# Performance work log

Measured on AMD Instinct MI355X. Metric: run time of the kernel, lower is better.

## Reference

```python
import jax, jax.numpy as jnp
import numpy as np


def setup_inputs() -> dict:
    key = jax.random.key(0)
    k1, k2, k3 = jax.random.split(key, 3)
    B, T, C = 4, 2048, 1024
    dim = C
    x = jax.random.normal(k1, (B, T, C), dtype=jnp.float32)
    # torch nn.Linear weight layout: [out_features, in_features], scaled like kaiming-uniform-ish
    w_qkv = jax.random.normal(k2, (3 * dim, dim), dtype=jnp.float32) * (1.0 / np.sqrt(dim))
    w_out = jax.random.normal(k3, (dim, dim), dtype=jnp.float32) * (1.0 / np.sqrt(dim))
    return {"x": x, "w_qkv": w_qkv, "w_out": w_out}


def reference(x, w_qkv, w_out):
    B, T, C = x.shape
    n_heads = 16
    head_dim = C // n_heads

    qkv = jnp.einsum("btc,dc->btd", x, w_qkv)  # [B,T,3C]
    q, k, v = jnp.split(qkv, 3, axis=-1)

    def split_heads(t):
        return t.reshape(B, T, n_heads, head_dim).transpose(0, 2, 1, 3)  # [B,H,T,hd]

    q, k, v = split_heads(q), split_heads(k), split_heads(v)

    scale = 1.0 / np.sqrt(head_dim).astype(np.float32)
    scores = jnp.einsum("bhqd,bhkd->bhqk", q, k) * scale  # [B,H,T,T]
    causal = jnp.tril(jnp.ones((T, T), dtype=bool))
    scores = jnp.where(causal, scores, jnp.finfo(scores.dtype).min)
    attn = jax.nn.softmax(scores, axis=-1)
    out = jnp.einsum("bhqk,bhkd->bhqd", attn, v)  # [B,H,T,hd]
    out = out.transpose(0, 2, 1, 3).reshape(B, T, C)
    return jnp.einsum("btc,dc->btd", out, w_out)
```

## Files before the change

kernel.cpp:

```cpp
#include <hip/hip_runtime.h>
#include <hip/hip_bf16.h>


typedef __attribute__((ext_vector_type(8))) short bf16x8;
typedef __attribute__((ext_vector_type(4))) float f32x4;
typedef __attribute__((ext_vector_type(16))) float f32x16;
typedef __attribute__((ext_vector_type(2))) unsigned uint2v;

#define GLOBAL_AS __attribute__((address_space(1)))
#define LDS_AS __attribute__((address_space(3)))

__device__ __forceinline__ unsigned short f2b_rne(float f) {
  unsigned u = __float_as_uint(f);
  unsigned r = u + 0x7fffu + ((u >> 16) & 1u);
  return (unsigned short)(r >> 16);
}

__device__ __forceinline__ unsigned cvt_pk_bf16(float lo, float hi) {
  unsigned r;
  asm("v_cvt_pk_bf16_f32 %0, %1, %2" : "=v"(r) : "v"(lo), "v"(hi));
  return r;
}

__device__ __forceinline__ void gload_lds16(const void* g, void* l) {
  __builtin_amdgcn_global_load_lds((const GLOBAL_AS void*)g, (LDS_AS void*)l, 16, 0, 0);
}

__global__ void f32_to_bf16_vec(const float* __restrict__ src,
                                unsigned short* __restrict__ dst, int n4) {
  int i = blockIdx.x * blockDim.x + threadIdx.x;
  int stride = gridDim.x * blockDim.x;
  for (; i < n4; i += stride) {
    float4 v = reinterpret_cast<const float4*>(src)[i];
    ushort4 o;
    o.x = f2b_rne(v.x); o.y = f2b_rne(v.y);
    o.z = f2b_rne(v.z); o.w = f2b_rne(v.w);
    reinterpret_cast<ushort4*>(dst)[i] = o;
  }
}

__global__ __launch_bounds__(256)
void v_transpose(const unsigned short* __restrict__ qkv,
                 unsigned short* __restrict__ vt) {
  __shared__ __align__(16) unsigned short Ts[64][64];
  const int tc = blockIdx.x, bh = blockIdx.y;
  const int b = bh >> 4, hed = bh & 15;
  const int t0 = tc * 64;
  const int tid = threadIdx.x;
  {
    const int r = tid >> 2, cb = (tid & 3) * 2;
    const unsigned short* src =
        qkv + (size_t)(b * 2048 + t0 + r) * 3072 + 2048 + hed * 64;
    bf16x8 v0 = *(const bf16x8*)(src + cb * 8);
    bf16x8 v1 = *(const bf16x8*)(src + cb * 8 + 8);
    *(bf16x8*)&Ts[r][(cb ^ (r & 7)) * 8] = v0;
    *(bf16x8*)&Ts[r][((cb + 1) ^ (r & 7)) * 8] = v1;
  }
  __syncthreads();
  const int d = tid >> 2;
  unsigned short* dst = vt + ((size_t)bh * 64 + d) * 2048 + t0;
#pragma unroll
  for (int tb2 = 0; tb2 < 2; ++tb2) {
    int tb = (tid & 3) * 2 + tb2;
    union { unsigned short s[8]; bf16x8 v; } o;
#pragma unroll
    for (int i = 0; i < 8; ++i) {
      int row = tb * 8 + i;
      o.s[i] = Ts[row][(((d >> 3) ^ (row & 7)) * 8) + (d & 7)];
    }
    *(bf16x8*)(dst + tb * 8) = o.v;
  }
}

template <int N, int OUT_BF16>
__global__ __launch_bounds__(512)
void gemm_big(const unsigned short* __restrict__ A,
              const unsigned short* __restrict__ B,
              void* __restrict__ Cout) {
  const int K = 1024;
  __shared__ __align__(16) unsigned short As[2][2][128 * 64];
  __shared__ __align__(16) unsigned short Bs[2][128 * 64];

  const int tid = threadIdx.x, wid = tid >> 6, lane = tid & 63;
  const int l31 = lane & 31, h = lane >> 5;
  const int NBX = N / 128;
  const int nwg8 = (int)gridDim.x >> 3;
  const int wgid = ((int)blockIdx.x & 7) * nwg8 + ((int)blockIdx.x >> 3);
  const int bx = wgid % NBX, by = wgid / NBX;
  const int m0 = by * 256, n0 = bx * 128;
  const int wr = wid >> 1, wc = wid & 1;

  auto stage = [&](int t, int buf) {
    const int k0 = t * 64;
    const int r8 = lane >> 3;
    const int blk = (lane & 7) ^ r8;
#pragma unroll
    for (int hh = 0; hh < 2; ++hh)
#pragma unroll
      for (int r = 0; r < 2; ++r) {
        int row = r * 64 + wid * 8 + r8;
        gload_lds16(A + (size_t)(m0 + hh * 128 + row) * K + k0 + blk * 8,
                    &As[buf][hh][r * 4096 + wid * 512]);
      }
#pragma unroll
    for (int r = 0; r < 2; ++r) {
      int row = r * 64 + wid * 8 + r8;
      gload_lds16(B + (size_t)(n0 + row) * K + k0 + blk * 8,
                  &Bs[buf][r * 4096 + wid * 512]);
    }
  };

  f32x16 acc[2][2] = {};

  stage(0, 0);

  int cur = 0;
  for (int t = 0; t < 16; ++t) {
    __builtin_amdgcn_s_barrier();
    if (t + 1 < 16) {
      stage(t + 1, cur ^ 1);
      asm volatile("s_waitcnt vmcnt(6)" ::: "memory");
    } else {
      asm volatile("s_waitcnt vmcnt(0)" ::: "memory");
    }
    __builtin_amdgcn_s_barrier();
    __builtin_amdgcn_sched_barrier(0);

    bf16x8 af[2][4], bfr[2][4];
#pragma unroll
    for (int mi = 0; mi < 2; ++mi) {
      int row = (wr & 1) * 64 + mi * 32 + l31;
#pragma unroll
      for (int ks = 0; ks < 4; ++ks) {
        int chunk = (ks * 2 + h) ^ (row & 7);
        af[mi][ks] = *(const bf16x8*)&As[cur][wr >> 1][row * 64 + chunk * 8];
      }
    }
#pragma unroll
    for (int ni = 0; ni < 2; ++ni) {
      int row = wc * 64 + ni * 32 + l31;
#pragma unroll
      for (int ks = 0; ks < 4; ++ks) {
        int chunk = (ks * 2 + h) ^ (row & 7);
        bfr[ni][ks] = *(const bf16x8*)&Bs[cur][row * 64 + chunk * 8];
      }
    }
    __builtin_amdgcn_s_setprio(1);
#pragma unroll
    for (int ks = 0; ks < 4; ++ks)
#pragma unroll
      for (int mi = 0; mi < 2; ++mi)
#pragma unroll
        for (int ni = 0; ni < 2; ++ni)
          acc[mi][ni] = __builtin_amdgcn_mfma_f32_32x32x16_bf16(
              af[mi][ks], bfr[ni][ks], acc[mi][ni], 0, 0, 0);
    __builtin_amdgcn_s_setprio(0);
    cur ^= 1;
  }

#pragma unroll
  for (int mi = 0; mi < 2; ++mi)
#pragma unroll
    for (int ni = 0; ni < 2; ++ni)
#pragma unroll
      for (int reg = 0; reg < 16; ++reg) {
        int row = m0 + wr * 64 + mi * 32 + (reg & 3) + 8 * (reg >> 2) + 4 * h;
        int col = n0 + wc * 64 + ni * 32 + l31;
        if (OUT_BF16)
          ((unsigned short*)Cout)[(size_t)row * N + col] =
              f2b_rne(acc[mi][ni][reg]);
        else
          ((float*)Cout)[(size_t)row * N + col] = acc[mi][ni][reg];
      }
}

__global__ __launch_bounds__(256, 2)
void attn_fwd(const unsigned short* __restrict__ qkv,
              const unsigned short* __restrict__ vt,
              unsigned short* __restrict__ out) {
  const int T = 2048, C3 = 3072;
  __shared__ __align__(16) unsigned short Ks[2][64][64];
  __shared__ __align__(16) unsigned short Vs[2][64][64];
  __shared__ float Bc[4][32];

  const int tid = threadIdx.x, w = tid >> 6, lane = tid & 63;
  const int l31 = lane & 31, h = lane >> 5;
  const int wgid = (blockIdx.x & 7) * 64 + (blockIdx.x >> 3);
  const int local = wgid & 63, xcd = wgid >> 6;
  const int qidx = local >> 3, bhl = local & 7;
  const int bh = xcd * 8 + bhl;
  const int qt = (qidx < 4) ? (7 - qidx) : (qidx - 4);
  const int b = bh >> 4, hed = bh & 15;
  const int qw = qt * 256 + w * 64;
  const size_t rowbase = (size_t)b * T * C3;
  const int hoff = hed * 64;
  const unsigned short* vbase = vt + (size_t)bh * 64 * 2048;
  const float c2 = 0.18033688f;

  auto stageK = [&](int kv0, int buf) {
#pragma unroll
    for (int pp = 0; pp < 2; ++pp) {
      int chunk = w * 2 + pp;
      int row = chunk * 8 + (lane >> 3);
      int blk = (lane & 7) ^ (lane >> 3);
      gload_lds16(
          qkv + rowbase + (size_t)(kv0 + row) * C3 + 1024 + hoff + blk * 8,
          &Ks[buf][chunk * 8][0]);
    }
  };
  auto stageV = [&](int kv0, int buf) {
#pragma unroll
    for (int pp = 0; pp < 2; ++pp) {
      int chunk = w * 2 + pp;
      int drow = chunk * 8 + (lane >> 3);
      int blk = (lane & 7) ^ (lane >> 3);
      gload_lds16(vbase + (size_t)drow * 2048 + kv0 + blk * 8,
                  &Vs[buf][chunk * 8][0]);
    }
  };

  bf16x8 qf0[4], qf1[4];
  {
    const unsigned short* qp0 =
        qkv + rowbase + (size_t)(qw + l31) * C3 + hoff + h * 8;
    const unsigned short* qp1 = qp0 + 32 * C3;
#pragma unroll
    for (int s = 0; s < 4; ++s) {
      qf0[s] = *(const bf16x8*)(qp0 + 16 * s);
      qf1[s] = *(const bf16x8*)(qp1 + 16 * s);
    }
  }

  f32x16 oacc0[2] = {}, oacc1[2] = {};
  float mr0 = -1e30f, mr1 = -1e30f, sum0 = 0.f, sum1 = 0.f;

  stageK(0, 0);
  stageV(0, 0);

  auto do_half = [&](f32x16 (&sacc)[2], int qx, float& mr, float& sm,
                     f32x16 (&oc)[2], int t, int kv0, int cur) {
    if (kv0 + 64 > qx) {
      int q_abs = qx + l31;
#pragma unroll
      for (int kt = 0; kt < 2; ++kt)
#pragma unroll
        for (int r = 0; r < 16; ++r) {
          int kv_abs = kv0 + kt * 32 + (r & 3) + 8 * (r >> 2) + 4 * h;
          if (kv_abs > q_abs) sacc[kt][r] = -1e30f;
        }
    }
    float mx[8];
#pragma unroll
    for (int g = 0; g < 8; ++g)
      mx[g] = fmaxf(fmaxf(sacc[g >> 2][(g & 3) * 4 + 0],
                          sacc[g >> 2][(g & 3) * 4 + 1]),
                    fmaxf(sacc[g >> 2][(g & 3) * 4 + 2],
                          sacc[g >> 2][(g & 3) * 4 + 3]));
    float tm = fmaxf(fmaxf(fmaxf(mx[0], mx[1]), fmaxf(mx[2], mx[3])),
                     fmaxf(fmaxf(mx[4], mx[5]), fmaxf(mx[6], mx[7])));
    tm = fmaxf(tm, __shfl_xor(tm, 32));
    if (t == 0) {
      mr = tm;
    } else if (!__all(tm <= mr + 16.0f)) {
      float mnew = fmaxf(mr, tm);
      float corr = __builtin_amdgcn_exp2f((mr - mnew) * c2);
      sm *= corr;
      if (h == 0) Bc[w][l31] = corr;
      mr = mnew;
      asm volatile("s_waitcnt lgkmcnt(0)" ::: "memory");
#pragma unroll
      for (int r = 0; r < 16; ++r) {
        float cr = Bc[w][(r & 3) + 8 * (r >> 2) + 4 * h];
        oc[0][r] *= cr;
        oc[1][r] *= cr;
      }
    }
    float m2 = mr * c2;
    float s0 = 0.f, s1 = 0.f, s2 = 0.f, s3 = 0.f;
#pragma unroll
    for (int kt = 0; kt < 2; ++kt)
#pragma unroll
      for (int r = 0; r < 16; r += 4) {
        float p0 = __builtin_amdgcn_exp2f(fmaf(sacc[kt][r + 0], c2, -m2));
        float p1 = __builtin_amdgcn_exp2f(fmaf(sacc[kt][r + 1], c2, -m2));
        float p2 = __builtin_amdgcn_exp2f(fmaf(sacc[kt][r + 2], c2, -m2));
        float p3 = __builtin_amdgcn_exp2f(fmaf(sacc[kt][r + 3], c2, -m2));
        sacc[kt][r + 0] = p0; sacc[kt][r + 1] = p1;
        sacc[kt][r + 2] = p2; sacc[kt][r + 3] = p3;
        s0 += p0; s1 += p1; s2 += p2; s3 += p3;
      }
    float sl = (s0 + s1) + (s2 + s3);
    sm += sl + __shfl_xor(sl, 32);
    unsigned pk[16];
#pragma unroll
    for (int kt = 0; kt < 2; ++kt)
#pragma unroll
      for (int r = 0; r < 16; r += 2)
        pk[kt * 8 + (r >> 1)] = cvt_pk_bf16(sacc[kt][r], sacc[kt][r + 1]);
    __builtin_amdgcn_s_setprio(1);
#pragma unroll
    for (int sg = 0; sg < 4; ++sg) {
      const int kt = sg >> 1, s = sg & 1;
      const int base = kt * 8 + 4 * s;
      uint2v r02 = __builtin_amdgcn_permlane32_swap(pk[base], pk[base + 2],
                                                    false, false);
      uint2v r13 = __builtin_amdgcn_permlane32_swap(pk[base + 1], pk[base + 3],
                                                    false, false);
      union { unsigned u[4]; bf16x8 v; } Afr;
      Afr.u[0] = r02.x; Afr.u[1] = r13.x;
      Afr.u[2] = r02.y; Afr.u[3] = r13.y;
#pragma unroll
      for (int dt = 0; dt < 2; ++dt) {
        int d = dt * 32 + l31;
        int blk = (2 * sg + h) ^ (d & 7);
        bf16x8 vf = *(const bf16x8*)&Vs[cur][d][blk * 8];
        oc[dt] = __builtin_amdgcn_mfma_f32_32x32x16_bf16(Afr.v, vf,
                                                         oc[dt], 0, 0, 0);
      }
    }
    __builtin_amdgcn_s_setprio(0);
  };

  int cur = 0;
  const int ntiles = 4 * qt + 4;
  for (int t = 0; t < ntiles; ++t) {
    const int kv0 = t * 64;
    __builtin_amdgcn_s_barrier();
    if (t + 1 < ntiles) {
      stageK(kv0 + 64, cur ^ 1);
      stageV(kv0 + 64, cur ^ 1);
      asm volatile("s_waitcnt vmcnt(4)" ::: "memory");
    } else {
      asm volatile("s_waitcnt vmcnt(0)" ::: "memory");
    }
    __builtin_amdgcn_s_barrier();
    __builtin_amdgcn_sched_barrier(0);

    if (kv0 <= qw) {
      f32x16 sacc0[2] = {}, sacc1[2] = {};
      __builtin_amdgcn_s_setprio(1);
#pragma unroll
      for (int s = 0; s < 4; ++s) {
#pragma unroll
        for (int kt = 0; kt < 2; ++kt) {
          int row = kt * 32 + l31;
          int blk = (2 * s + h) ^ (row & 7);
          bf16x8 kf = *(const bf16x8*)&Ks[cur][row][blk * 8];
          sacc0[kt] = __builtin_amdgcn_mfma_f32_32x32x16_bf16(kf, qf0[s],
                                                              sacc0[kt], 0, 0, 0);
          sacc1[kt] = __builtin_amdgcn_mfma_f32_32x32x16_bf16(kf, qf1[s],
                                                              sacc1[kt], 0, 0, 0);
        }
      }
      __builtin_amdgcn_s_setprio(0);
      do_half(sacc0, qw, mr0, sum0, oacc0, t, kv0, cur);
      do_half(sacc1, qw + 32, mr1, sum1, oacc1, t, kv0, cur);
    }
    cur ^= 1;
  }

#pragma unroll
  for (int X = 0; X < 2; ++X) {
    float sm = X ? sum1 : sum0;
    if (h == 0) Bc[w][l31] = 1.0f / sm;
    asm volatile("s_waitcnt lgkmcnt(0)" ::: "memory");
#pragma unroll
    for (int r = 0; r < 16; ++r) {
      int ql = (r & 3) + 8 * (r >> 2) + 4 * h;
      float inv = Bc[w][ql];
      int q_abs = qw + 32 * X + ql;
#pragma unroll
      for (int dt = 0; dt < 2; ++dt) {
        float v = (X ? oacc1 : oacc0)[dt][r] * inv;
        out[(size_t)(b * T + q_abs) * 1024 + hoff + dt * 32 + l31] =
            f2b_rne(v);
      }
    }
    __builtin_amdgcn_s_barrier();
  }
}

extern "C" void kernel_launch(void* const* d_in, const int* in_sizes, int n_in,
                              void* d_out, int out_size, void* d_ws,
                              size_t ws_size, hipStream_t stream) {
  const float* x = (const float*)d_in[0];
  const float* w_qkv = (const float*)d_in[1];
  const float* w_out = (const float*)d_in[2];
  float* out = (float*)d_out;

  const int M = 8192, C = 1024, C3 = 3072;

  unsigned short* xb = (unsigned short*)d_ws;
  unsigned short* wqkvb = xb + (size_t)M * C;
  unsigned short* woutb = wqkvb + (size_t)C3 * C;
  unsigned short* qkv = woutb + (size_t)C * C;
  unsigned short* vtb = qkv + (size_t)M * C3;
  unsigned short* attno = xb;

  f32_to_bf16_vec<<<1024, 256, 0, stream>>>(x, xb, M * C / 4);
  f32_to_bf16_vec<<<512, 256, 0, stream>>>(w_qkv, wqkvb, C3 * C / 4);
  f32_to_bf16_vec<<<256, 256, 0, stream>>>(w_out, woutb, C * C / 4);

  gemm_big<3072, 1><<<768, 512, 0, stream>>>(xb, wqkvb, qkv);

  v_transpose<<<dim3(32, 64), 256, 0, stream>>>(qkv, vtb);

  attn_fwd<<<512, 256, 0, stream>>>(qkv, vtb, attno);

  gemm_big<1024, 0><<<256, 512, 0, stream>>>(attno, woutb, out);
}
```

Baseline: 189.8 us.

## Use persistent attention blocks with atomic work queue; fuse conversion kernels

```diff
diff --git a/kernel.cpp b/kernel.cpp
--- a/kernel.cpp
+++ b/kernel.cpp
@@ -26,16 +26,34 @@
   __builtin_amdgcn_global_load_lds((const GLOBAL_AS void*)g, (LDS_AS void*)l, 16, 0, 0);
 }
 
-__global__ void f32_to_bf16_vec(const float* __restrict__ src,
-                                unsigned short* __restrict__ dst, int n4) {
+__global__ void fused_convert(const float* __restrict__ x,
+                              const float* __restrict__ wqkv,
+                              const float* __restrict__ wout,
+                              unsigned short* __restrict__ xb,
+                              unsigned short* __restrict__ wqkvb,
+                              unsigned short* __restrict__ woutb,
+                              int* __restrict__ ctr) {
+  if (blockIdx.x == 0 && threadIdx.x == 0) *ctr = 0;
+  const int nx = 8192 * 1024 / 4, nq = 3072 * 1024 / 4, nw = 1024 * 1024 / 4;
+  const int ntot = nx + nq + nw;
   int i = blockIdx.x * blockDim.x + threadIdx.x;
   int stride = gridDim.x * blockDim.x;
-  for (; i < n4; i += stride) {
-    float4 v = reinterpret_cast<const float4*>(src)[i];
+  for (; i < ntot; i += stride) {
+    const float* src;
+    unsigned short* dst;
+    int j = i;
+    if (j < nx) {
+      src = x; dst = xb;
+    } else if ((j -= nx) < nq) {
+      src = wqkv; dst = wqkvb;
+    } else {
+      j -= nq; src = wout; dst = woutb;
+    }
+    float4 v = reinterpret_cast<const float4*>(src)[j];
     ushort4 o;
     o.x = f2b_rne(v.x); o.y = f2b_rne(v.y);
     o.z = f2b_rne(v.z); o.w = f2b_rne(v.w);
-    reinterpret_cast<ushort4*>(dst)[i] = o;
+    reinterpret_cast<ushort4*>(dst)[j] = o;
   }
 }
 
@@ -177,206 +195,213 @@
 __global__ __launch_bounds__(256, 2)
 void attn_fwd(const unsigned short* __restrict__ qkv,
               const unsigned short* __restrict__ vt,
-              unsigned short* __restrict__ out) {
+              unsigned short* __restrict__ out,
+              int* __restrict__ ctr) {
   const int T = 2048, C3 = 3072;
   __shared__ __align__(16) unsigned short Ks[2][64][64];
   __shared__ __align__(16) unsigned short Vs[2][64][64];
   __shared__ float Bc[4][32];
+  __shared__ int sIdx;
 
   const int tid = threadIdx.x, w = tid >> 6, lane = tid & 63;
   const int l31 = lane & 31, h = lane >> 5;
-  const int wgid = (blockIdx.x & 7) * 64 + (blockIdx.x >> 3);
-  const int local = wgid & 63, xcd = wgid >> 6;
-  const int qidx = local >> 3, bhl = local & 7;
-  const int bh = xcd * 8 + bhl;
-  const int qt = (qidx < 4) ? (7 - qidx) : (qidx - 4);
-  const int b = bh >> 4, hed = bh & 15;
-  const int qw = qt * 256 + w * 64;
-  const size_t rowbase = (size_t)b * T * C3;
-  const int hoff = hed * 64;
-  const unsigned short* vbase = vt + (size_t)bh * 64 * 2048;
   const float c2 = 0.18033688f;
 
-  auto stageK = [&](int kv0, int buf) {
-#pragma unroll
-    for (int pp = 0; pp < 2; ++pp) {
-      int chunk = w * 2 + pp;
-      int row = chunk * 8 + (lane >> 3);
-      int blk = (lane & 7) ^ (lane >> 3);
-      gload_lds16(
-          qkv + rowbase + (size_t)(kv0 + row) * C3 + 1024 + hoff + blk * 8,
-          &Ks[buf][chunk * 8][0]);
-    }
-  };
-  auto stageV = [&](int kv0, int buf) {
-#pragma unroll
-    for (int pp = 0; pp < 2; ++pp) {
-      int chunk = w * 2 + pp;
-      int drow = chunk * 8 + (lane >> 3);
-      int blk = (lane & 7) ^ (lane >> 3);
-      gload_lds16(vbase + (size_t)drow * 2048 + kv0 + blk * 8,
-                  &Vs[buf][chunk * 8][0]);
-    }
-  };
-
-  bf16x8 qf0[4], qf1[4];
-  {
-    const unsigned short* qp0 =
-        qkv + rowbase + (size_t)(qw + l31) * C3 + hoff + h * 8;
-    const unsigned short* qp1 = qp0 + 32 * C3;
-#pragma unroll
-    for (int s = 0; s < 4; ++s) {
-      qf0[s] = *(const bf16x8*)(qp0 + 16 * s);
-      qf1[s] = *(const bf16x8*)(qp1 + 16 * s);
-    }
-  }
-
-  f32x16 oacc0[2] = {}, oacc1[2] = {};
-  float mr0 = -1e30f, mr1 = -1e30f, sum0 = 0.f, sum1 = 0.f;
-
-  stageK(0, 0);
-  stageV(0, 0);
-
-  auto do_half = [&](f32x16 (&sacc)[2], int qx, float& mr, float& sm,
-                     f32x16 (&oc)[2], int t, int kv0, int cur) {
-    if (kv0 + 64 > qx) {
-      int q_abs = qx + l31;
+  for (;;) {
+    if (tid == 0) sIdx = atomicAdd(ctr, 1);
+    __syncthreads();
+    const int idx = sIdx;
+    if (idx >= 512) break;
+    const int qt = 7 - (idx >> 6);
+    const int bh = idx & 63;
+    const int b = bh >> 4, hed = bh & 15;
+    const int qw = qt * 256 + w * 64;
+    const size_t rowbase = (size_t)b * T * C3;
+    const int hoff = hed * 64;
+    const unsigned short* vbase = vt + (size_t)bh * 64 * 2048;
+
+    auto stageK = [&](int kv0, int buf) {
+#pragma unroll
+      for (int pp = 0; pp < 2; ++pp) {
+        int chunk = w * 2 + pp;
+        int row = chunk * 8 + (lane >> 3);
+        int blk = (lane & 7) ^ (lane >> 3);
+        gload_lds16(
+            qkv + rowbase + (size_t)(kv0 + row) * C3 + 1024 + hoff + blk * 8,
+            &Ks[buf][chunk * 8][0]);
+      }
+    };
+    auto stageV = [&](int kv0, int buf) {
+#pragma unroll
+      for (int pp = 0; pp < 2; ++pp) {
+        int chunk = w * 2 + pp;
+        int drow = chunk * 8 + (lane >> 3);
+        int blk = (lane & 7) ^ (lane >> 3);
+        gload_lds16(vbase + (size_t)drow * 2048 + kv0 + blk * 8,
+                    &Vs[buf][chunk * 8][0]);
+      }
+    };
+
+    bf16x8 qf0[4], qf1[4];
+    {
+      const unsigned short* qp0 =
+          qkv + rowbase + (size_t)(qw + l31) * C3 + hoff + h * 8;
+      const unsigned short* qp1 = qp0 + 32 * C3;
+#pragma unroll
+      for (int s = 0; s < 4; ++s) {
+        qf0[s] = *(const bf16x8*)(qp0 + 16 * s);
+        qf1[s] = *(const bf16x8*)(qp1 + 16 * s);
+      }
+    }
+
+    f32x16 oacc0[2] = {}, oacc1[2] = {};
+    float mr0 = -1e30f, mr1 = -1e30f, sum0 = 0.f, sum1 = 0.f;
+
+    stageK(0, 0);
+    stageV(0, 0);
+
+    auto do_half = [&](f32x16 (&sacc)[2], int qx, float& mr, float& sm,
+                       f32x16 (&oc)[2], int t, int kv0, int cur) {
+      if (kv0 + 64 > qx) {
+        int q_abs = qx + l31;
+#pragma unroll
+        for (int kt = 0; kt < 2; ++kt)
+#pragma unroll
+          for (int r = 0; r < 16; ++r) {
+            int kv_abs = kv0 + kt * 32 + (r & 3) + 8 * (r >> 2) + 4 * h;
+            if (kv_abs > q_abs) sacc[kt][r] = -1e30f;
+          }
+      }
+      float mx[8];
+#pragma unroll
+      for (int g = 0; g < 8; ++g)
+        mx[g] = fmaxf(fmaxf(sacc[g >> 2][(g & 3) * 4 + 0],
+                            sacc[g >> 2][(g & 3) * 4 + 1]),
+                      fmaxf(sacc[g >> 2][(g & 3) * 4 + 2],
+                            sacc[g >> 2][(g & 3) * 4 + 3]));
+      float tm = fmaxf(fmaxf(fmaxf(mx[0], mx[1]), fmaxf(mx[2], mx[3])),
+                       fmaxf(fmaxf(mx[4], mx[5]), fmaxf(mx[6], mx[7])));
+      tm = fmaxf(tm, __shfl_xor(tm, 32));
+      if (t == 0) {
+        mr = tm;
+      } else if (!__all(tm <= mr + 16.0f)) {
+        float mnew = fmaxf(mr, tm);
+        float corr = __builtin_amdgcn_exp2f((mr - mnew) * c2);
+        sm *= corr;
+        if (h == 0) Bc[w][l31] = corr;
+        mr = mnew;
+        asm volatile("s_waitcnt lgkmcnt(0)" ::: "memory");
+#pragma unroll
+        for (int r = 0; r < 16; ++r) {
+          float cr = Bc[w][(r & 3) + 8 * (r >> 2) + 4 * h];
+          oc[0][r] *= cr;
+          oc[1][r] *= cr;
+        }
+      }
+      float m2 = mr * c2;
+      float s0 = 0.f, s1 = 0.f, s2 = 0.f, s3 = 0.f;
 #pragma unroll
       for (int kt = 0; kt < 2; ++kt)
 #pragma unroll
-        for (int r = 0; r < 16; ++r) {
-          int kv_abs = kv0 + kt * 32 + (r & 3) + 8 * (r >> 2) + 4 * h;
-          if (kv_abs > q_abs) sacc[kt][r] = -1e30f;
+        for (int r = 0; r < 16; r += 4) {
+          float p0 = __builtin_amdgcn_exp2f(fmaf(sacc[kt][r + 0], c2, -m2));
+          float p1 = __builtin_amdgcn_exp2f(fmaf(sacc[kt][r + 1], c2, -m2));
+          float p2 = __builtin_amdgcn_exp2f(fmaf(sacc[kt][r + 2], c2, -m2));
+          float p3 = __builtin_amdgcn_exp2f(fmaf(sacc[kt][r + 3], c2, -m2));
+          sacc[kt][r + 0] = p0; sacc[kt][r + 1] = p1;
+          sacc[kt][r + 2] = p2; sacc[kt][r + 3] = p3;
+          s0 += p0; s1 += p1; s2 += p2; s3 += p3;
         }
-    }
-    float mx[8];
-#pragma unroll
-    for (int g = 0; g < 8; ++g)
-      mx[g] = fmaxf(fmaxf(sacc[g >> 2][(g & 3) * 4 + 0],
-                          sacc[g >> 2][(g & 3) * 4 + 1]),
-                    fmaxf(sacc[g >> 2][(g & 3) * 4 + 2],
-                          sacc[g >> 2][(g & 3) * 4 + 3]));
-    float tm = fmaxf(fmaxf(fmaxf(mx[0], mx[1]), fmaxf(mx[2], mx[3])),
-                     fmaxf(fmaxf(mx[4], mx[5]), fmaxf(mx[6], mx[7])));
-    tm = fmaxf(tm, __shfl_xor(tm, 32));
-    if (t == 0) {
-      mr = tm;
-    } else if (!__all(tm <= mr + 16.0f)) {
-      float mnew = fmaxf(mr, tm);
-      float corr = __builtin_amdgcn_exp2f((mr - mnew) * c2);
-      sm *= corr;
-      if (h == 0) Bc[w][l31] = corr;
-      mr = mnew;
+      float sl = (s0 + s1) + (s2 + s3);
+      sm += sl + __shfl_xor(sl, 32);
+      unsigned pk[16];
+#pragma unroll
+      for (int kt = 0; kt < 2; ++kt)
+#pragma unroll
+        for (int r = 0; r < 16; r += 2)
+          pk[kt * 8 + (r >> 1)] = cvt_pk_bf16(sacc[kt][r], sacc[kt][r + 1]);
+      __builtin_amdgcn_s_setprio(1);
+#pragma unroll
+      for (int sg = 0; sg < 4; ++sg) {
+        const int kt = sg >> 1, s = sg & 1;
+        const int base = kt * 8 + 4 * s;
+        uint2v r02 = __builtin_amdgcn_permlane32_swap(pk[base], pk[base + 2],
+                                                      false, false);
+        uint2v r13 = __builtin_amdgcn_permlane32_swap(pk[base + 1], pk[base + 3],
+                                                      false, false);
+        union { unsigned u[4]; bf16x8 v; } Afr;
+        Afr.u[0] = r02.x; Afr.u[1] = r13.x;
+        Afr.u[2] = r02.y; Afr.u[3] = r13.y;
+#pragma unroll
+        for (int dt = 0; dt < 2; ++dt) {
+          int d = dt * 32 + l31;
+          int blk = (2 * sg + h) ^ (d & 7);
+          bf16x8 vf = *(const bf16x8*)&Vs[cur][d][blk * 8];
+          oc[dt] = __builtin_amdgcn_mfma_f32_32x32x16_bf16(Afr.v, vf,
+                                                           oc[dt], 0, 0, 0);
+        }
+      }
+      __builtin_amdgcn_s_setprio(0);
+    };
+
+    int cur = 0;
+    const int ntiles = 4 * qt + 4;
+    for (int t = 0; t < ntiles; ++t) {
+      const int kv0 = t * 64;
+      __builtin_amdgcn_s_barrier();
+      if (t + 1 < ntiles) {
+        stageK(kv0 + 64, cur ^ 1);
+        stageV(kv0 + 64, cur ^ 1);
+        asm volatile("s_waitcnt vmcnt(4)" ::: "memory");
+      } else {
+        asm volatile("s_waitcnt vmcnt(0)" ::: "memory");
+      }
+      __builtin_amdgcn_s_barrier();
+      __builtin_amdgcn_sched_barrier(0);
+
+      if (kv0 <= qw) {
+        f32x16 sacc0[2] = {}, sacc1[2] = {};
+        __builtin_amdgcn_s_setprio(1);
+#pragma unroll
+        for (int s = 0; s < 4; ++s) {
+#pragma unroll
+          for (int kt = 0; kt < 2; ++kt) {
+            int row = kt * 32 + l31;
+            int blk = (2 * s + h) ^ (row & 7);
+            bf16x8 kf = *(const bf16x8*)&Ks[cur][row][blk * 8];
+            sacc0[kt] = __builtin_amdgcn_mfma_f32_32x32x16_bf16(
+                kf, qf0[s], sacc0[kt], 0, 0, 0);
+            sacc1[kt] = __builtin_amdgcn_mfma_f32_32x32x16_bf16(
+                kf, qf1[s], sacc1[kt], 0, 0, 0);
+          }
+        }
+        __builtin_amdgcn_s_setprio(0);
+        do_half(sacc0, qw, mr0, sum0, oacc0, t, kv0, cur);
+        do_half(sacc1, qw + 32, mr1, sum1, oacc1, t, kv0, cur);
+      }
+      cur ^= 1;
+    }
+
+#pragma unroll
+    for (int X = 0; X < 2; ++X) {
+      float sm = X ? sum1 : sum0;
+      if (h == 0) Bc[w][l31] = 1.0f / sm;
       asm volatile("s_waitcnt lgkmcnt(0)" ::: "memory");
 #pragma unroll
       for (int r = 0; r < 16; ++r) {
-        float cr = Bc[w][(r & 3) + 8 * (r >> 2) + 4 * h];
-        oc[0][r] *= cr;
-        oc[1][r] *= cr;
-      }
-    }
-    float m2 = mr * c2;
-    float s0 = 0.f, s1 = 0.f, s2 = 0.f, s3 = 0.f;
-#pragma unroll
-    for (int kt = 0; kt < 2; ++kt)
-#pragma unroll
-      for (int r = 0; r < 16; r += 4) {
-        float p0 = __builtin_amdgcn_exp2f(fmaf(sacc[kt][r + 0], c2, -m2));
-        float p1 = __builtin_amdgcn_exp2f(fmaf(sacc[kt][r + 1], c2, -m2));
-        float p2 = __builtin_amdgcn_exp2f(fmaf(sacc[kt][r + 2], c2, -m2));
-        float p3 = __builtin_amdgcn_exp2f(fmaf(sacc[kt][r + 3], c2, -m2));
-        sacc[kt][r + 0] = p0; sacc[kt][r + 1] = p1;
-        sacc[kt][r + 2] = p2; sacc[kt][r + 3] = p3;
-        s0 += p0; s1 += p1; s2 += p2; s3 += p3;
-      }
-    float sl = (s0 + s1) + (s2 + s3);
-    sm += sl + __shfl_xor(sl, 32);
-    unsigned pk[16];
-#pragma unroll
-    for (int kt = 0; kt < 2; ++kt)
-#pragma unroll
-      for (int r = 0; r < 16; r += 2)
-        pk[kt * 8 + (r >> 1)] = cvt_pk_bf16(sacc[kt][r], sacc[kt][r + 1]);
-    __builtin_amdgcn_s_setprio(1);
-#pragma unroll
-    for (int sg = 0; sg < 4; ++sg) {
-      const int kt = sg >> 1, s = sg & 1;
-      const int base = kt * 8 + 4 * s;
-      uint2v r02 = __builtin_amdgcn_permlane32_swap(pk[base], pk[base + 2],
-                                                    false, false);
-      uint2v r13 = __builtin_amdgcn_permlane32_swap(pk[base + 1], pk[base + 3],
-                                                    false, false);
-      union { unsigned u[4]; bf16x8 v; } Afr;
-      Afr.u[0] = r02.x; Afr.u[1] = r13.x;
-      Afr.u[2] = r02.y; Afr.u[3] = r13.y;
-#pragma unroll
-      for (int dt = 0; dt < 2; ++dt) {
-        int d = dt * 32 + l31;
-        int blk = (2 * sg + h) ^ (d & 7);
-        bf16x8 vf = *(const bf16x8*)&Vs[cur][d][blk * 8];
-        oc[dt] = __builtin_amdgcn_mfma_f32_32x32x16_bf16(Afr.v, vf,
-                                                         oc[dt], 0, 0, 0);
-      }
-    }
-    __builtin_amdgcn_s_setprio(0);
-  };
-
-  int cur = 0;
-  const int ntiles = 4 * qt + 4;
-  for (int t = 0; t < ntiles; ++t) {
-    const int kv0 = t * 64;
-    __builtin_amdgcn_s_barrier();
-    if (t + 1 < ntiles) {
-      stageK(kv0 + 64, cur ^ 1);
-      stageV(kv0 + 64, cur ^ 1);
-      asm volatile("s_waitcnt vmcnt(4)" ::: "memory");
-    } else {
-      asm volatile("s_waitcnt vmcnt(0)" ::: "memory");
-    }
-    __builtin_amdgcn_s_barrier();
-    __builtin_amdgcn_sched_barrier(0);
-
-    if (kv0 <= qw) {
-      f32x16 sacc0[2] = {}, sacc1[2] = {};
-      __builtin_amdgcn_s_setprio(1);
-#pragma unroll
-      for (int s = 0; s < 4; ++s) {
-#pragma unroll
-        for (int kt = 0; kt < 2; ++kt) {
-          int row = kt * 32 + l31;
-          int blk = (2 * s + h) ^ (row & 7);
-          bf16x8 kf = *(const bf16x8*)&Ks[cur][row][blk * 8];
-          sacc0[kt] = __builtin_amdgcn_mfma_f32_32x32x16_bf16(kf, qf0[s],
-                                                              sacc0[kt], 0, 0, 0);
-          sacc1[kt] = __builtin_amdgcn_mfma_f32_32x32x16_bf16(kf, qf1[s],
-                                                              sacc1[kt], 0, 0, 0);
+        int ql = (r & 3) + 8 * (r >> 2) + 4 * h;
+        float inv = Bc[w][ql];
+        int q_abs = qw + 32 * X + ql;
+#pragma unroll
+        for (int dt = 0; dt < 2; ++dt) {
+          float v = (X ? oacc1 : oacc0)[dt][r] * inv;
+          out[(size_t)(b * T + q_abs) * 1024 + hoff + dt * 32 + l31] =
+              f2b_rne(v);
         }
       }
-      __builtin_amdgcn_s_setprio(0);
-      do_half(sacc0, qw, mr0, sum0, oacc0, t, kv0, cur);
-      do_half(sacc1, qw + 32, mr1, sum1, oacc1, t, kv0, cur);
-    }
-    cur ^= 1;
-  }
-
-#pragma unroll
-  for (int X = 0; X < 2; ++X) {
-    float sm = X ? sum1 : sum0;
-    if (h == 0) Bc[w][l31] = 1.0f / sm;
-    asm volatile("s_waitcnt lgkmcnt(0)" ::: "memory");
-#pragma unroll
-    for (int r = 0; r < 16; ++r) {
-      int ql = (r & 3) + 8 * (r >> 2) + 4 * h;
-      float inv = Bc[w][ql];
-      int q_abs = qw + 32 * X + ql;
-#pragma unroll
-      for (int dt = 0; dt < 2; ++dt) {
-        float v = (X ? oacc1 : oacc0)[dt][r] * inv;
-        out[(size_t)(b * T + q_abs) * 1024 + hoff + dt * 32 + l31] =
-            f2b_rne(v);
-      }
-    }
-    __builtin_amdgcn_s_barrier();
+      __builtin_amdgcn_s_barrier();
+    }
+    __syncthreads();
   }
 }
 
@@ -396,16 +421,16 @@
   unsigned short* qkv = woutb + (size_t)C * C;
   unsigned short* vtb = qkv + (size_t)M * C3;
   unsigned short* attno = xb;
-
-  f32_to_bf16_vec<<<1024, 256, 0, stream>>>(x, xb, M * C / 4);
-  f32_to_bf16_vec<<<512, 256, 0, stream>>>(w_qkv, wqkvb, C3 * C / 4);
-  f32_to_bf16_vec<<<256, 256, 0, stream>>>(w_out, woutb, C * C / 4);
+  int* ctr = (int*)(vtb + (size_t)M * C);
+
+  fused_convert<<<2048, 256, 0, stream>>>(x, w_qkv, w_out, xb, wqkvb, woutb,
+                                          ctr);
 
   gemm_big<3072, 1><<<768, 512, 0, stream>>>(xb, wqkvb, qkv);
 
   v_transpose<<<dim3(32, 64), 256, 0, stream>>>(qkv, vtb);
 
-  attn_fwd<<<512, 256, 0, stream>>>(qkv, vtb, attno);
+  attn_fwd<<<384, 256, 0, stream>>>(qkv, vtb, attno, ctr);
 
   gemm_big<1024, 0><<<256, 512, 0, stream>>>(attno, woutb, out);
 }
```

After: 204.3 us. +7.6%, slower.
